# Kernel optimization log

Hardware: AMD Instinct MI355X
Metric: run time of the kernel (lower is better)

## Reference

```python
import jax, jax.numpy as jnp
import numpy as np

N = 50000
E = 800000
G = 256          # number of graphs in the batch
F_IN = 128
H1, D1 = 12, 32  # conv1: heads, out-per-head (concat -> 384)
H2, D2 = 1, 64   # conv2: single head
NEG_SLOPE = 0.2


def setup_inputs() -> dict:
    key = jax.random.key(0)
    ks = jax.random.split(key, 12)
    x = jax.random.normal(ks[0], (N, F_IN), dtype=jnp.float32)
    edge_index = jax.random.randint(ks[1], (2, E), 0, N, dtype=jnp.int64)
    batch = jnp.sort(jax.random.randint(ks[2], (N,), 0, G, dtype=jnp.int64))
    # conv1 params (Glorot-ish scaling)
    W1 = jax.random.normal(ks[3], (F_IN, H1 * D1), dtype=jnp.float32) * (1.0 / np.sqrt(F_IN))
    att_src1 = jax.random.normal(ks[4], (H1, D1), dtype=jnp.float32) * (1.0 / np.sqrt(D1))
    att_dst1 = jax.random.normal(ks[5], (H1, D1), dtype=jnp.float32) * (1.0 / np.sqrt(D1))
    bias1 = jnp.zeros((H1 * D1,), dtype=jnp.float32)
    # conv2 params
    W2 = jax.random.normal(ks[6], (H1 * D1, H2 * D2), dtype=jnp.float32) * (1.0 / np.sqrt(H1 * D1))
    att_src2 = jax.random.normal(ks[7], (H2, D2), dtype=jnp.float32) * (1.0 / np.sqrt(D2))
    att_dst2 = jax.random.normal(ks[8], (H2, D2), dtype=jnp.float32) * (1.0 / np.sqrt(D2))
    bias2 = jnp.zeros((H2 * D2,), dtype=jnp.float32)
    return {"x": x, "edge_index": edge_index, "batch": batch,
            "W1": W1, "att_src1": att_src1, "att_dst1": att_dst1, "bias1": bias1,
            "W2": W2, "att_src2": att_src2, "att_dst2": att_dst2, "bias2": bias2}


def gat_conv(x, src, dst, W, att_src, att_dst, bias, heads, d_out):
    # x: [N, F] -> h: [N, heads, d_out]
    h = (x @ W).reshape(N, heads, d_out)
    # per-node attention halves: [N, heads]
    a_src = jnp.einsum('nhd,hd->nh', h, att_src)
    a_dst = jnp.einsum('nhd,hd->nh', h, att_dst)
    # per-edge logits (edges include self-loops): [Etot, heads]
    e = jax.nn.leaky_relu(a_src[src] + a_dst[dst], NEG_SLOPE)
    # segment softmax over incoming edges of each destination node
    m = jax.ops.segment_max(e, dst, num_segments=N)          # [N, heads]
    e = jnp.exp(e - m[dst])
    s = jax.ops.segment_sum(e, dst, num_segments=N)          # [N, heads]
    alpha = e / s[dst]
    # weighted aggregation: [N, heads, d_out]
    out = jax.ops.segment_sum(alpha[:, :, None] * h[src], dst, num_segments=N)
    return out.reshape(N, heads * d_out) + bias


def reference(x, edge_index, batch, W1, att_src1, att_dst1, bias1,
              W2, att_src2, att_dst2, bias2):
    # add self-loops (PyG GATConv default add_self_loops=True)
    loops = jnp.arange(N, dtype=edge_index.dtype)
    src = jnp.concatenate([edge_index[0], loops])
    dst = jnp.concatenate([edge_index[1], loops])

    h = jax.nn.relu(gat_conv(x, src, dst, W1, att_src1, att_dst1, bias1, H1, D1))
    h = gat_conv(h, src, dst, W2, att_src2, att_dst2, bias2, H2, D2)

    # global mean pool over graphs
    sums = jax.ops.segment_sum(h, batch, num_segments=G)                 # [G, 64]
    cnts = jax.ops.segment_sum(jnp.ones((N,), h.dtype), batch, num_segments=G)
    return sums / jnp.maximum(cnts, 1.0)[:, None]
```

## Files before the change

kernel.cpp:

```cpp
#include <hip/hip_runtime.h>

#define N_NODES 50000
#define N_EDGES 800000
#define ETOT (N_EDGES + N_NODES)
#define G_GRAPHS 256
#define F_IN 128
#define H1 12
#define D1 32
#define C1 (H1*D1)
#define C2 64
#define NEG 0.2f
#define SCAN_B 1024
#define NBLK_SCAN ((N_NODES + SCAN_B - 1)/SCAN_B)

using bf16x8  = __attribute__((ext_vector_type(8))) short;
using ushort8 = __attribute__((ext_vector_type(8))) unsigned short;
using f32x4   = __attribute__((ext_vector_type(4))) float;

__device__ __forceinline__ float lrelu(float x){ return x > 0.f ? x : NEG*x; }
__device__ __forceinline__ unsigned short f2bf(float f){
  unsigned u = __float_as_uint(f);
  u += 0x7fffu + ((u >> 16) & 1u);
  return (unsigned short)(u >> 16);
}
__device__ __forceinline__ float bf2f(unsigned short h){
  return __uint_as_float(((unsigned)h) << 16);
}
__device__ __forceinline__ float wexp(float l){ return __expf(fminf(l, 30.f)); }

#define B_CAST ((N_NODES*F_IN/4 + 255)/256)
#define B_W1   ((F_IN*C1 + 255)/256)
#define B_W2   ((C1*C2 + 255)/256)
#define B_WAB  ((32*F_IN + 255)/256)
__global__ void prep_kernel(const float* __restrict__ x, const float* __restrict__ W1,
    const float* __restrict__ W2, const float* __restrict__ att_src,
    const float* __restrict__ att_dst, unsigned short* __restrict__ xb,
    unsigned short* __restrict__ w1t, unsigned short* __restrict__ w2t,
    unsigned short* __restrict__ wAb){
  int b = blockIdx.x, tid = threadIdx.x;
  if (b < B_CAST){
    int base = (b*256 + tid)*4;
    if (base >= N_NODES*F_IN) return;
    float4 v = *(const float4*)(x + base);
    ushort4 o; o.x=f2bf(v.x); o.y=f2bf(v.y); o.z=f2bf(v.z); o.w=f2bf(v.w);
    *(ushort4*)(xb + base) = o;
  } else if (b < B_CAST + B_W1){
    int i = (b - B_CAST)*256 + tid;
    if (i >= F_IN*C1) return;
    int n = i / F_IN, k = i % F_IN;
    w1t[i] = f2bf(W1[(size_t)k*C1 + n]);
  } else if (b < B_CAST + B_W1 + B_W2){
    int i = (b - B_CAST - B_W1)*256 + tid;
    if (i >= C1*C2) return;
    int n = i / C1, k = i % C1;
    w2t[i] = f2bf(W2[(size_t)k*C2 + n]);
  } else {
    int i = (b - B_CAST - B_W1 - B_W2)*256 + tid;
    if (i >= 32*F_IN) return;
    int c = i >> 7, k = i & 127;
    float v = 0.f;
    if (c < 12){
      #pragma unroll
      for (int dd=0; dd<D1; ++dd) v += W1[(size_t)k*C1 + c*D1 + dd] * att_src[c*D1 + dd];
    } else if (c < 24){
      int h = c - 12;
      #pragma unroll
      for (int dd=0; dd<D1; ++dd) v += W1[(size_t)k*C1 + h*D1 + dd] * att_dst[h*D1 + dd];
    }
    wAb[i] = f2bf(v);
  }
}

template<int BM,int BN,int WM,int WN,bool F32OUT>
__global__ __launch_bounds__(256) void gemm_mfma(const unsigned short* __restrict__ A,
    const unsigned short* __restrict__ Bt, void* __restrict__ Cv,
    int M, int N, int K){
  constexpr int BK = 32;
  __shared__ unsigned short As2[4][BM][8];
  __shared__ unsigned short Bs2[4][BN][8];
  const int tid  = threadIdx.x;
  const int wid  = tid >> 6, lane = tid & 63;
  constexpr int NWX = BN / WN;
  const int wrow = (wid / NWX) * WM, wcol = (wid % NWX) * WN;
  constexpr int MR = WM/16, NR = WN/16;
  const int row0 = blockIdx.x * BM, col0 = blockIdx.y * BN;
  const int r = lane & 15, koct = lane >> 4;
  f32x4 acc[MR][NR];
  #pragma unroll
  for (int m=0;m<MR;m++)
    #pragma unroll
    for (int n=0;n<NR;n++) acc[m][n] = f32x4{0.f,0.f,0.f,0.f};

  for (int k0 = 0; k0 < K; k0 += BK){
    for (int s = tid; s < BM*8; s += 256){
      int rr = s >> 3, cc = (s & 7) * 4;
      int gr = row0 + rr;
      ushort4 v = (gr < M) ? *(const ushort4*)(A + (size_t)gr*K + k0 + cc)
                           : ushort4{0,0,0,0};
      *(ushort4*)(&As2[cc>>3][rr][cc&7]) = v;
    }
    for (int s = tid; s < BN*8; s += 256){
      int rr = s >> 3, cc = (s & 7) * 4;
      ushort4 v = *(const ushort4*)(Bt + (size_t)(col0+rr)*K + k0 + cc);
      *(ushort4*)(&Bs2[cc>>3][rr][cc&7]) = v;
    }
    __syncthreads();
    bf16x8 af[MR], bq[NR];
    #pragma unroll
    for (int m=0;m<MR;m++) af[m] = *(const bf16x8*)(&As2[koct][wrow + m*16 + r][0]);
    #pragma unroll
    for (int n=0;n<NR;n++) bq[n] = *(const bf16x8*)(&Bs2[koct][wcol + n*16 + r][0]);
    #pragma unroll
    for (int m=0;m<MR;m++)
      #pragma unroll
      for (int n=0;n<NR;n++)
        acc[m][n] = __builtin_amdgcn_mfma_f32_16x16x32_bf16(af[m], bq[n], acc[m][n], 0,0,0);
    __syncthreads();
  }
  #pragma unroll
  for (int m=0;m<MR;m++){
    #pragma unroll
    for (int rr=0; rr<4; rr++){
      int grow = row0 + wrow + m*16 + koct*4 + rr;
      if (grow < M){
        #pragma unroll
        for (int n=0;n<NR;n++){
          if constexpr (F32OUT)
            ((float*)Cv)[(size_t)grow*N + col0 + wcol + n*16 + r] = acc[m][n][rr];
          else
            ((unsigned short*)Cv)[(size_t)grow*N + col0 + wcol + n*16 + r] = f2bf(acc[m][n][rr]);
        }
      }
    }
  }
}

#define EGRID ((ETOT + 255)/256)
#define NGRID ((N_NODES + 255)/256)
__global__ void count_cnt_kernel(const int* __restrict__ ei, const int* __restrict__ batch,
                                 int* __restrict__ counts, int* __restrict__ cnt){
  if ((int)blockIdx.x < EGRID){
    int e = blockIdx.x*256 + threadIdx.x;
    if (e >= ETOT) return;
    int d = (e < N_EDGES) ? ei[N_EDGES + e] : (e - N_EDGES);
    atomicAdd(&counts[d], 1);
  } else {
    int n = (blockIdx.x - EGRID)*256 + threadIdx.x;
    if (n < N_NODES) atomicAdd(&cnt[batch[n]], 1);
  }
}
__global__ __launch_bounds__(SCAN_B) void scan_pass1(const int* __restrict__ counts,
    int* __restrict__ excl, int* __restrict__ bsum){
  __shared__ int sdata[SCAN_B];
  int i = blockIdx.x*SCAN_B + threadIdx.x;
  int v = (i < N_NODES) ? counts[i] : 0;
  sdata[threadIdx.x] = v;
  __syncthreads();
  for (int off=1; off<SCAN_B; off<<=1){
    int t = (threadIdx.x >= off) ? sdata[threadIdx.x-off] : 0;
    __syncthreads();
    sdata[threadIdx.x] += t;
    __syncthreads();
  }
  if (i < N_NODES) excl[i] = sdata[threadIdx.x] - v;
  if (threadIdx.x == SCAN_B-1) bsum[blockIdx.x] = sdata[SCAN_B-1];
}
__global__ void scan_pass3(int* __restrict__ rowptr, const int* __restrict__ bsum,
                           int* __restrict__ cursor){
  __shared__ int carry_s;
  int sblk = blockIdx.x >> 2;
  if (threadIdx.x == 0){
    int c = 0;
    for (int b=0; b<sblk; ++b) c += bsum[b];
    carry_s = c;
  }
  __syncthreads();
  int i = blockIdx.x*256 + (int)threadIdx.x;
  if (i < N_NODES){
    int r = rowptr[i] + carry_s;
    rowptr[i] = r; cursor[i] = r;
  }
  if (i == N_NODES) rowptr[N_NODES] = ETOT;
}
__global__ void scatter_kernel(const int* __restrict__ ei, int* __restrict__ cursor,
                               int* __restrict__ csr_src, int* __restrict__ csr_dst){
  int e = blockIdx.x*blockDim.x + threadIdx.x;
  if (e >= ETOT) return;
  int s, d;
  if (e < N_EDGES){ s = ei[e]; d = ei[N_EDGES + e]; } else { s = d = e - N_EDGES; }
  int slot = atomicAdd(&cursor[d], 1);
  csr_src[slot] = s;
  csr_dst[slot] = d;
}

__global__ void wprep_kernel(const int* __restrict__ csr, const int* __restrict__ csrd,
                             const float* __restrict__ asd, unsigned short* __restrict__ walpha){
  int j = blockIdx.x*256 + threadIdx.x;
  if (j >= ETOT) return;
  int s = csr[j], d = csrd[j];
  float4 s0 = *(const float4*)(asd + (size_t)s*32);
  float4 s1 = *(const float4*)(asd + (size_t)s*32 + 4);
  float4 s2 = *(const float4*)(asd + (size_t)s*32 + 8);
  float4 d0 = *(const float4*)(asd + (size_t)d*32 + 12);
  float4 d1 = *(const float4*)(asd + (size_t)d*32 + 16);
  float4 d2 = *(const float4*)(asd + (size_t)d*32 + 20);
  float as[12] = {s0.x,s0.y,s0.z,s0.w, s1.x,s1.y,s1.z,s1.w, s2.x,s2.y,s2.z,s2.w};
  float ad[12] = {d0.x,d0.y,d0.z,d0.w, d1.x,d1.y,d1.z,d1.w, d2.x,d2.y,d2.z,d2.w};
  unsigned short wb[12];
  #pragma unroll
  for (int h=0;h<12;h++) wb[h] = f2bf(wexp(lrelu(as[h] + ad[h])));
  unsigned short* wp = walpha + (size_t)j*12;
  *(ushort4*)(wp)   = ushort4{wb[0],wb[1],wb[2],wb[3]};
  *(ushort4*)(wp+4) = ushort4{wb[4],wb[5],wb[6],wb[7]};
  *(ushort4*)(wp+8) = ushort4{wb[8],wb[9],wb[10],wb[11]};
}

__global__ __launch_bounds__(512, 4) void agg1h_kernel(const int* __restrict__ rowptr,
    const int* __restrict__ csr, const unsigned short* __restrict__ xb,
    const unsigned short* __restrict__ walpha, const unsigned short* __restrict__ w1t,
    const unsigned short* __restrict__ w2t, const float* __restrict__ bias1,
    const float* __restrict__ att_src2, const float* __restrict__ att_dst2,
    unsigned short* __restrict__ h2, float* __restrict__ asrc2, float* __restrict__ adst2){
  constexpr int ROWE = 6*F_IN + 8;
  constexpr int WROW = 32*12 + 4;
  constexpr int ROWR = 192 + 8;
  __shared__ unsigned short agg[16*ROWE];
  __shared__ float wlds[16][WROW];

  unsigned short* reluLDS = (unsigned short*)&wlds[0][0];
  float* red = (float*)&agg[0];

  const int tid  = threadIdx.x;
  const int wv   = tid >> 6;
  const int lane = tid & 63;
  const int half = lane >> 5;
  const int t32  = lane & 31;
  const int base = lane & 32;
  const int slot = wv*2 + half;
  const int d    = blockIdx.x*16 + slot;
  const int r0 = rowptr[d], r1 = rowptr[d+1];

  float acc[12][4];
  #pragma unroll
  for (int h=0;h<12;h++)
    #pragma unroll
    for (int i=0;i<4;i++) acc[h][i] = 0.f;
  float ss[12];
  #pragma unroll
  for (int h=0;h<12;h++) ss[h] = 0.f;

  for (int c0 = r0; c0 < r1; c0 += 32){
    int nc = min(32, r1 - c0);
    int s_st = 0;
    if (t32 < nc){
      int j = c0 + t32;
      s_st = csr[j];
      const unsigned short* wp = walpha + (size_t)j*12;
      ushort4 u0 = *(const ushort4*)(wp);
      ushort4 u1 = *(const ushort4*)(wp+4);
      ushort4 u2 = *(const ushort4*)(wp+8);
      float w[12] = {bf2f(u0.x),bf2f(u0.y),bf2f(u0.z),bf2f(u0.w),
                     bf2f(u1.x),bf2f(u1.y),bf2f(u1.z),bf2f(u1.w),
                     bf2f(u2.x),bf2f(u2.y),bf2f(u2.z),bf2f(u2.w)};
      #pragma unroll
      for (int h=0;h<12;h++) ss[h] += w[h];
      *(float4*)(&wlds[slot][t32*12 + 0]) = float4{w[0],w[1],w[2],w[3]};
      *(float4*)(&wlds[slot][t32*12 + 4]) = float4{w[4],w[5],w[6],w[7]};
      *(float4*)(&wlds[slot][t32*12 + 8]) = float4{w[8],w[9],w[10],w[11]};
    }
    __builtin_amdgcn_wave_barrier();
    int sA = __shfl(s_st, base + 0);
    ushort4 xA = *(const ushort4*)(xb + (size_t)sA*F_IN + t32*4);
    ushort4 xB = {0,0,0,0}, xC = {0,0,0,0};
    if (nc > 1){
      int sB = __shfl(s_st, base + 1);
      xB = *(const ushort4*)(xb + (size_t)sB*F_IN + t32*4);
    }
    if (nc > 2){
      int sC = __shfl(s_st, base + 2);
      xC = *(const ushort4*)(xb + (size_t)sC*F_IN + t32*4);
    }
    for (int e = 0; e < nc; ++e){
      ushort4 cx = xA;
      xA = xB; xB = xC;
      if (e + 3 < nc){
        int sN = __shfl(s_st, base + e + 3);
        xC = *(const ushort4*)(xb + (size_t)sN*F_IN + t32*4);
      }
      float4 w0 = *(const float4*)(&wlds[slot][e*12 + 0]);
      float4 w1 = *(const float4*)(&wlds[slot][e*12 + 4]);
      float4 w2 = *(const float4*)(&wlds[slot][e*12 + 8]);
      float xf[4] = {bf2f(cx.x), bf2f(cx.y), bf2f(cx.z), bf2f(cx.w)};
      float w[12] = {w0.x,w0.y,w0.z,w0.w, w1.x,w1.y,w1.z,w1.w, w2.x,w2.y,w2.z,w2.w};
      #pragma unroll
      for (int h=0;h<12;h++)
        #pragma unroll
        for (int i=0;i<4;i++) acc[h][i] += w[h]*xf[i];
    }
    __builtin_amdgcn_wave_barrier();
  }

  #pragma unroll
  for (int h=0;h<12;h++){
    #pragma unroll
    for (int off=16; off; off>>=1) ss[h] += __shfl_xor(ss[h], off);
  }
  float inv[12];
  #pragma unroll
  for (int h=0;h<12;h++) inv[h] = 1.f / ss[h];

  const int er = lane & 15, eq = lane >> 4;
  f32x4 h2acc = {0.f,0.f,0.f,0.f};
  #pragma unroll
  for (int hf = 0; hf < 2; ++hf){
    __syncthreads();
    #pragma unroll
    for (int h = 0; h < 6; ++h){
      int hh = hf*6 + h;
      ushort4 v;
      v.x = f2bf(acc[hh][0]*inv[hh]); v.y = f2bf(acc[hh][1]*inv[hh]);
      v.z = f2bf(acc[hh][2]*inv[hh]); v.w = f2bf(acc[hh][3]*inv[hh]);
      *(ushort4*)(&agg[slot*ROWE + h*F_IN + t32*4]) = v;
    }
    __syncthreads();
    for (int tt = wv; tt < 12; tt += 8){
      int h = tt >> 1, nb = tt & 1;
      int hh = hf*6 + h;
      f32x4 c = {0.f,0.f,0.f,0.f};
      #pragma unroll
      for (int kk=0; kk<4; ++kk){
        bf16x8 af = *(const bf16x8*)(&agg[er*ROWE + h*F_IN + kk*32 + eq*8]);
        bf16x8 bq = *(const bf16x8*)(w1t + (size_t)(hh*32 + nb*16 + er)*F_IN + kk*32 + eq*8);
        c = __builtin_amdgcn_mfma_f32_16x16x32_bf16(af, bq, c, 0,0,0);
      }
      int lcol = tt*16 + er;
      float bv = bias1[hf*192 + lcol];
      #pragma unroll
      for (int rr=0; rr<4; ++rr){
        int row = eq*4 + rr;
        reluLDS[row*ROWR + lcol] = f2bf(fmaxf(c[rr] + bv, 0.f));
      }
    }
    __syncthreads();
    if (wv < 4){
      #pragma unroll
      for (int kk=0; kk<6; ++kk){
        bf16x8 af = *(const bf16x8*)(&reluLDS[er*ROWR + kk*32 + eq*8]);
        bf16x8 bq = *(const bf16x8*)(w2t + (size_t)(wv*16 + er)*C1 + hf*192 + kk*32 + eq*8);
        h2acc = __builtin_amdgcn_mfma_f32_16x16x32_bf16(af, bq, h2acc, 0,0,0);
      }
    }
  }
  __syncthreads();

  if (wv < 4){
    float attS = att_src2[wv*16 + er];
    float attD = att_dst2[wv*16 + er];
    float psum[4], pdum[4];
    #pragma unroll
    for (int rr=0; rr<4; ++rr){
      int row = eq*4 + rr;
      int gn = blockIdx.x*16 + row;
      h2[(size_t)gn*C2 + wv*16 + er] = f2bf(h2acc[rr]);
      psum[rr] = h2acc[rr]*attS;
      pdum[rr] = h2acc[rr]*attD;
    }
    #pragma unroll
    for (int rr=0; rr<4; ++rr){
      #pragma unroll
      for (int off=8; off; off>>=1){
        psum[rr] += __shfl_xor(psum[rr], off);
        pdum[rr] += __shfl_xor(pdum[rr], off);
      }
    }
    if (er == 0){
      #pragma unroll
      for (int rr=0; rr<4; ++rr){
        int row = eq*4 + rr;
        red[(wv*16 + row)*2 + 0] = psum[rr];
        red[(wv*16 + row)*2 + 1] = pdum[rr];
      }
    }
  }
  __syncthreads();
  if (tid < 32){
    int row = tid >> 1, which = tid & 1;
    float v = red[row*2+which] + red[(16+row)*2+which] + red[(32+row)*2+which] + red[(48+row)*2+which];
    int gn = blockIdx.x*16 + row;
    if (which == 0) asrc2[gn] = v; else adst2[gn] = v;
  }
}

__global__ __launch_bounds__(256) void agg2s_kernel(const int* __restrict__ rowptr,
    const int* __restrict__ csr, const unsigned short* __restrict__ h2,
    const float* __restrict__ asrc, const float* __restrict__ adst,
    const float* __restrict__ bias, const int* __restrict__ batch,
    float* __restrict__ pool){
  const int tid  = threadIdx.x;
  const int slot = tid >> 4;
  const int t16  = tid & 15;
  const int base = ((tid & 63) >> 4) * 16;
  const int d    = blockIdx.x*16 + slot;
  const int r0 = rowptr[d], r1 = rowptr[d+1];
  const float ad = adst[d];

  float ssp = 0.f;
  float a0=0.f, a1=0.f, a2=0.f, a3=0.f;

  for (int c0 = r0; c0 < r1; c0 += 16){
    int nc = min(16, r1 - c0);
    int s_st = 0; float w_st = 0.f;
    if (t16 < nc){
      s_st = csr[c0 + t16];
      w_st = wexp(lrelu(asrc[s_st] + ad));
      ssp += w_st;
    }
    int sA = __shfl(s_st, base + 0);
    ushort4 xA = *(const ushort4*)(h2 + (size_t)sA*C2 + t16*4);
    ushort4 xB = {0,0,0,0}, xC = {0,0,0,0};
    if (nc > 1){
      int sB = __shfl(s_st, base + 1);
      xB = *(const ushort4*)(h2 + (size_t)sB*C2 + t16*4);
    }
    if (nc > 2){
      int sC = __shfl(s_st, base + 2);
      xC = *(const ushort4*)(h2 + (size_t)sC*C2 + t16*4);
    }
    for (int e = 0; e < nc; ++e){
      ushort4 cx = xA;
      xA = xB; xB = xC;
      if (e + 3 < nc){
        int sN = __shfl(s_st, base + e + 3);
        xC = *(const ushort4*)(h2 + (size_t)sN*C2 + t16*4);
      }
      float w = __shfl(w_st, base + e);
      a0 += w*bf2f(cx.x);
      a1 += w*bf2f(cx.y);
      a2 += w*bf2f(cx.z);
      a3 += w*bf2f(cx.w);
    }
  }
  #pragma unroll
  for (int off=8; off; off>>=1) ssp += __shfl_xor(ssp, off);
  float inv = 1.f / ssp;
  int g = batch[d];
  int fb = t16*4;
  atomicAdd(&pool[g*C2 + fb+0], a0*inv + bias[fb+0]);
  atomicAdd(&pool[g*C2 + fb+1], a1*inv + bias[fb+1]);
  atomicAdd(&pool[g*C2 + fb+2], a2*inv + bias[fb+2]);
  atomicAdd(&pool[g*C2 + fb+3], a3*inv + bias[fb+3]);
}

__global__ void finalize_kernel(const float* __restrict__ sums, const int* __restrict__ cnt,
                                float* __restrict__ out){
  int i = blockIdx.x*blockDim.x + threadIdx.x;
  if (i >= G_GRAPHS*C2) return;
  int g = i >> 6;
  out[i] = sums[i] / fmaxf((float)cnt[g], 1.f);
}

extern "C" void kernel_launch(void* const* d_in, const int* in_sizes, int n_in,
                              void* d_out, int out_size, void* d_ws, size_t ws_size,
                              hipStream_t stream) {
  const float* x        = (const float*)d_in[0];
  const int*   ei       = (const int*)  d_in[1];
  const int*   batch    = (const int*)  d_in[2];
  const float* W1       = (const float*)d_in[3];
  const float* att_src1 = (const float*)d_in[4];
  const float* att_dst1 = (const float*)d_in[5];
  const float* bias1    = (const float*)d_in[6];
  const float* W2       = (const float*)d_in[7];
  const float* att_src2 = (const float*)d_in[8];
  const float* att_dst2 = (const float*)d_in[9];
  const float* bias2    = (const float*)d_in[10];
  float* out = (float*)d_out;

  char* ws = (char*)d_ws;
  size_t o = 0;
  auto alloc = [&](size_t bytes)->size_t{ size_t r=o; o=(o+bytes+255)&~(size_t)255; return r; };

  size_t xb_o     = alloc((size_t)N_NODES*F_IN*2);
  size_t w1t_o    = alloc((size_t)C1*F_IN*2);
  size_t w2t_o    = alloc((size_t)C2*C1*2);
  size_t wab_o    = alloc((size_t)32*F_IN*2);
  size_t asd_o    = alloc((size_t)N_NODES*32*4);
  size_t h2_o     = alloc((size_t)N_NODES*C2*2);
  size_t asrc2_o  = alloc((size_t)N_NODES*4);
  size_t adst2_o  = alloc((size_t)N_NODES*4);
  size_t walpha_o = alloc((size_t)ETOT*12*2);
  size_t zero_beg = o;
  size_t counts_o = alloc((size_t)N_NODES*4);
  size_t pool_o   = alloc((size_t)G_GRAPHS*C2*4);
  size_t cnt_o    = alloc((size_t)G_GRAPHS*4);
  size_t zero_end = o;
  size_t rowptr_o = alloc((size_t)(N_NODES+1)*4);
  size_t bsum_o   = alloc((size_t)NBLK_SCAN*4);
  size_t cursor_o = alloc((size_t)N_NODES*4);
  size_t csr_o    = alloc((size_t)ETOT*4);
  size_t csrd_o   = alloc((size_t)ETOT*4);

  unsigned short* xb    = (unsigned short*)(ws + xb_o);
  unsigned short* w1t   = (unsigned short*)(ws + w1t_o);
  unsigned short* w2t   = (unsigned short*)(ws + w2t_o);
  unsigned short* wab   = (unsigned short*)(ws + wab_o);
  float* asd    = (float*)(ws + asd_o);
  unsigned short* h2b   = (unsigned short*)(ws + h2_o);
  float* asrc2  = (float*)(ws + asrc2_o);
  float* adst2  = (float*)(ws + adst2_o);
  unsigned short* walpha = (unsigned short*)(ws + walpha_o);
  int*   counts = (int*)  (ws + counts_o);
  float* poolf  = (float*)(ws + pool_o);
  int*   cnt    = (int*)  (ws + cnt_o);
  int*   rowptr = (int*)  (ws + rowptr_o);
  int*   bsum   = (int*)  (ws + bsum_o);
  int*   cursor = (int*)  (ws + cursor_o);
  int*   csrsrc = (int*)  (ws + csr_o);
  int*   csrdst = (int*)  (ws + csrd_o);

  hipMemsetAsync(ws + zero_beg, 0, zero_end - zero_beg, stream);

  const int TPB = 256;

  prep_kernel<<<B_CAST + B_W1 + B_W2 + B_WAB, TPB, 0, stream>>>(
      x, W1, W2, att_src1, att_dst1, xb, w1t, w2t, wab);

  count_cnt_kernel<<<EGRID + NGRID, TPB, 0, stream>>>(ei, batch, counts, cnt);
  scan_pass1<<<NBLK_SCAN, SCAN_B, 0, stream>>>(counts, rowptr, bsum);
  scan_pass3<<<(N_NODES + 1 + 255)/256, TPB, 0, stream>>>(rowptr, bsum, cursor);
  scatter_kernel<<<EGRID, TPB, 0, stream>>>(ei, cursor, csrsrc, csrdst);

  gemm_mfma<64,32,32,16,true><<<dim3((N_NODES+63)/64, 1), 256, 0, stream>>>(xb, wab, asd, N_NODES, 32, F_IN);
  wprep_kernel<<<EGRID, TPB, 0, stream>>>(csrsrc, csrdst, asd, walpha);
  agg1h_kernel<<<N_NODES/16, 512, 0, stream>>>(rowptr, csrsrc, xb, walpha, w1t, w2t,
                                               bias1, att_src2, att_dst2, h2b, asrc2, adst2);
  agg2s_kernel<<<(N_NODES+15)/16, TPB, 0, stream>>>(rowptr, csrsrc, h2b, asrc2, adst2, bias2, batch, poolf);

  finalize_kernel<<<(G_GRAPHS*C2 + TPB-1)/TPB, TPB, 0, stream>>>(poolf, cnt, out);
}
```

Baseline: 415.0 us.

## Group destination nodes by in-degree and precompute layer-2 edge weights

Adds a degree histogram, a bin scan and a placement pass that build a permutation sorting nodes by in-degree. Both aggregation kernels now process nodes in that order, so the 16 nodes in a block have similar edge counts and wave-level load imbalance shrinks. Layer-2 attention weights are also precomputed per edge in a separate kernel instead of being computed inside agg2s. The cost is four extra launches, extra ETOT-sized traffic for w2a, and scattered output writes and lost locality because nodes are no longer contiguous per block.

```diff
diff --git a/kernel.cpp b/kernel.cpp
--- a/kernel.cpp
+++ b/kernel.cpp
@@ -12,6 +12,7 @@
 #define NEG 0.2f
 #define SCAN_B 1024
 #define NBLK_SCAN ((N_NODES + SCAN_B - 1)/SCAN_B)
+#define NBINS 128
 
 using bf16x8  = __attribute__((ext_vector_type(8))) short;
 using ushort8 = __attribute__((ext_vector_type(8))) unsigned short;
@@ -193,6 +194,30 @@
   csr_dst[slot] = d;
 }
 
+__global__ void hist_kernel(const int* __restrict__ counts, int* __restrict__ hist){
+  __shared__ int lh[NBINS];
+  if (threadIdx.x < NBINS) lh[threadIdx.x] = 0;
+  __syncthreads();
+  int d = blockIdx.x*256 + threadIdx.x;
+  if (d < N_NODES) atomicAdd(&lh[min(counts[d], NBINS-1)], 1);
+  __syncthreads();
+  if (threadIdx.x < NBINS && lh[threadIdx.x]) atomicAdd(&hist[threadIdx.x], lh[threadIdx.x]);
+}
+__global__ void binscan_kernel(const int* __restrict__ hist, int* __restrict__ cursor2){
+  if (threadIdx.x == 0){
+    int acc = 0;
+    for (int b=0; b<NBINS; ++b){ int t = hist[b]; cursor2[b] = acc; acc += t; }
+  }
+}
+__global__ void place_kernel(const int* __restrict__ counts, int* __restrict__ cursor2,
+                             int* __restrict__ perm){
+  int d = blockIdx.x*256 + threadIdx.x;
+  if (d >= N_NODES) return;
+  int bin = min(counts[d], NBINS-1);
+  int slot = atomicAdd(&cursor2[bin], 1);
+  perm[slot] = d;
+}
+
 __global__ void wprep_kernel(const int* __restrict__ csr, const int* __restrict__ csrd,
                              const float* __restrict__ asd, unsigned short* __restrict__ walpha){
   int j = blockIdx.x*256 + threadIdx.x;
@@ -215,8 +240,17 @@
   *(ushort4*)(wp+8) = ushort4{wb[8],wb[9],wb[10],wb[11]};
 }
 
+__global__ void wprep2_kernel(const int* __restrict__ csr, const int* __restrict__ csrd,
+                              const float* __restrict__ asrc, const float* __restrict__ adst,
+                              float* __restrict__ w2a){
+  int j = blockIdx.x*256 + threadIdx.x;
+  if (j >= ETOT) return;
+  w2a[j] = wexp(lrelu(asrc[csr[j]] + adst[csrd[j]]));
+}
+
 __global__ __launch_bounds__(512, 4) void agg1h_kernel(const int* __restrict__ rowptr,
-    const int* __restrict__ csr, const unsigned short* __restrict__ xb,
+    const int* __restrict__ csr, const int* __restrict__ perm,
+    const unsigned short* __restrict__ xb,
     const unsigned short* __restrict__ walpha, const unsigned short* __restrict__ w1t,
     const unsigned short* __restrict__ w2t, const float* __restrict__ bias1,
     const float* __restrict__ att_src2, const float* __restrict__ att_dst2,
@@ -226,6 +260,7 @@
   constexpr int ROWR = 192 + 8;
   __shared__ unsigned short agg[16*ROWE];
   __shared__ float wlds[16][WROW];
+  __shared__ int pblk[16];
 
   unsigned short* reluLDS = (unsigned short*)&wlds[0][0];
   float* red = (float*)&agg[0];
@@ -237,7 +272,10 @@
   const int t32  = lane & 31;
   const int base = lane & 32;
   const int slot = wv*2 + half;
-  const int d    = blockIdx.x*16 + slot;
+
+  if (tid < 16) pblk[tid] = perm[blockIdx.x*16 + tid];
+  __syncthreads();
+  const int d = pblk[slot];
   const int r0 = rowptr[d], r1 = rowptr[d+1];
 
   float acc[12][4];
@@ -360,7 +398,7 @@
     #pragma unroll
     for (int rr=0; rr<4; ++rr){
       int row = eq*4 + rr;
-      int gn = blockIdx.x*16 + row;
+      int gn = pblk[row];
       h2[(size_t)gn*C2 + wv*16 + er] = f2bf(h2acc[rr]);
       psum[rr] = h2acc[rr]*attS;
       pdum[rr] = h2acc[rr]*attD;
@@ -386,23 +424,25 @@
   if (tid < 32){
     int row = tid >> 1, which = tid & 1;
     float v = red[row*2+which] + red[(16+row)*2+which] + red[(32+row)*2+which] + red[(48+row)*2+which];
-    int gn = blockIdx.x*16 + row;
+    int gn = pblk[row];
     if (which == 0) asrc2[gn] = v; else adst2[gn] = v;
   }
 }
 
 __global__ __launch_bounds__(256) void agg2s_kernel(const int* __restrict__ rowptr,
-    const int* __restrict__ csr, const unsigned short* __restrict__ h2,
-    const float* __restrict__ asrc, const float* __restrict__ adst,
+    const int* __restrict__ csr, const int* __restrict__ perm,
+    const unsigned short* __restrict__ h2, const float* __restrict__ w2a,
     const float* __restrict__ bias, const int* __restrict__ batch,
     float* __restrict__ pool){
+  __shared__ int pblk[16];
   const int tid  = threadIdx.x;
   const int slot = tid >> 4;
   const int t16  = tid & 15;
   const int base = ((tid & 63) >> 4) * 16;
-  const int d    = blockIdx.x*16 + slot;
+  if (tid < 16) pblk[tid] = perm[blockIdx.x*16 + tid];
+  __syncthreads();
+  const int d = pblk[slot];
   const int r0 = rowptr[d], r1 = rowptr[d+1];
-  const float ad = adst[d];
 
   float ssp = 0.f;
   float a0=0.f, a1=0.f, a2=0.f, a3=0.f;
@@ -412,7 +452,7 @@
     int s_st = 0; float w_st = 0.f;
     if (t16 < nc){
       s_st = csr[c0 + t16];
-      w_st = wexp(lrelu(asrc[s_st] + ad));
+      w_st = w2a[c0 + t16];
       ssp += w_st;
     }
     int sA = __shfl(s_st, base + 0);
@@ -488,14 +528,18 @@
   size_t asrc2_o  = alloc((size_t)N_NODES*4);
   size_t adst2_o  = alloc((size_t)N_NODES*4);
   size_t walpha_o = alloc((size_t)ETOT*12*2);
+  size_t w2a_o    = alloc((size_t)ETOT*4);
+  size_t perm_o   = alloc((size_t)N_NODES*4);
   size_t zero_beg = o;
   size_t counts_o = alloc((size_t)N_NODES*4);
   size_t pool_o   = alloc((size_t)G_GRAPHS*C2*4);
   size_t cnt_o    = alloc((size_t)G_GRAPHS*4);
+  size_t hist_o   = alloc((size_t)NBINS*4);
   size_t zero_end = o;
   size_t rowptr_o = alloc((size_t)(N_NODES+1)*4);
   size_t bsum_o   = alloc((size_t)NBLK_SCAN*4);
   size_t cursor_o = alloc((size_t)N_NODES*4);
+  size_t cursor2_o= alloc((size_t)NBINS*4);
   size_t csr_o    = alloc((size_t)ETOT*4);
   size_t csrd_o   = alloc((size_t)ETOT*4);
 
@@ -508,12 +552,16 @@
   float* asrc2  = (float*)(ws + asrc2_o);
   float* adst2  = (float*)(ws + adst2_o);
   unsigned short* walpha = (unsigned short*)(ws + walpha_o);
+  float* w2a    = (float*)(ws + w2a_o);
+  int*   perm   = (int*)  (ws + perm_o);
   int*   counts = (int*)  (ws + counts_o);
   float* poolf  = (float*)(ws + pool_o);
   int*   cnt    = (int*)  (ws + cnt_o);
+  int*   hist   = (int*)  (ws + hist_o);
   int*   rowptr = (int*)  (ws + rowptr_o);
   int*   bsum   = (int*)  (ws + bsum_o);
   int*   cursor = (int*)  (ws + cursor_o);
+  int*   cursor2= (int*)  (ws + cursor2_o);
   int*   csrsrc = (int*)  (ws + csr_o);
   int*   csrdst = (int*)  (ws + csrd_o);
 
@@ -528,12 +576,16 @@
   scan_pass1<<<NBLK_SCAN, SCAN_B, 0, stream>>>(counts, rowptr, bsum);
   scan_pass3<<<(N_NODES + 1 + 255)/256, TPB, 0, stream>>>(rowptr, bsum, cursor);
   scatter_kernel<<<EGRID, TPB, 0, stream>>>(ei, cursor, csrsrc, csrdst);
+  hist_kernel<<<NGRID, TPB, 0, stream>>>(counts, hist);
+  binscan_kernel<<<1, 64, 0, stream>>>(hist, cursor2);
+  place_kernel<<<NGRID, TPB, 0, stream>>>(counts, cursor2, perm);
 
   gemm_mfma<64,32,32,16,true><<<dim3((N_NODES+63)/64, 1), 256, 0, stream>>>(xb, wab, asd, N_NODES, 32, F_IN);
   wprep_kernel<<<EGRID, TPB, 0, stream>>>(csrsrc, csrdst, asd, walpha);
-  agg1h_kernel<<<N_NODES/16, 512, 0, stream>>>(rowptr, csrsrc, xb, walpha, w1t, w2t,
+  agg1h_kernel<<<N_NODES/16, 512, 0, stream>>>(rowptr, csrsrc, perm, xb, walpha, w1t, w2t,
                                                bias1, att_src2, att_dst2, h2b, asrc2, adst2);
-  agg2s_kernel<<<(N_NODES+15)/16, TPB, 0, stream>>>(rowptr, csrsrc, h2b, asrc2, adst2, bias2, batch, poolf);
+  wprep2_kernel<<<EGRID, TPB, 0, stream>>>(csrsrc, csrdst, asrc2, adst2, w2a);
+  agg2s_kernel<<<(N_NODES+15)/16, TPB, 0, stream>>>(rowptr, csrsrc, perm, h2b, w2a, bias2, batch, poolf);
 
   finalize_kernel<<<(G_GRAPHS*C2 + TPB-1)/TPB, TPB, 0, stream>>>(poolf, cnt, out);
 }
```

Result: slower. 546.0 us (+31.6%).
